# Performance work log

Hardware: AMD Instinct MI355X
Metric: run time of the kernel (lower is better)

Reference implementation:

```python
import jax, jax.numpy as jnp
import numpy as np

NUM_ROUTING = 3

def _squash(s):
    # squared_norm * s / ((1 + squared_norm) * sqrt(squared_norm)), norm over last dim
    sn = jnp.sum(s * s, axis=-1, keepdims=True)
    return sn * s / ((1.0 + sn) * jnp.sqrt(sn))

def setup_inputs() -> dict:
    key = jax.random.key(0)
    kx, kw = jax.random.split(key)
    B, IN_CAPS, IN_DIM, OUT_CAPS, OUT_DIM = 64, 8192, 8, 8, 16
    x = jax.random.normal(kx, (B, IN_CAPS, IN_DIM), dtype=jnp.float32)
    W = 0.01 * jax.random.normal(kw, (IN_CAPS, OUT_CAPS, IN_DIM, OUT_DIM), dtype=jnp.float32)
    return {"x": x, "W": W}

def reference(x, W):
    # x: [B, in_caps, in_dim]; W: [in_caps, out_caps, in_dim, out_dim]
    u_hat = jnp.einsum('ijnm,bin->bijm', W, x)          # [B, i, j, m]
    temp_u_hat = jax.lax.stop_gradient(u_hat)           # detach, routing uses no grads
    B, I, J = x.shape[0], W.shape[0], W.shape[1]
    b = jnp.zeros((B, I, J), dtype=x.dtype)
    for _ in range(NUM_ROUTING - 1):
        c = jax.nn.softmax(b, axis=2)                   # over out_caps j
        s = jnp.einsum('bij,bijm->bjm', c, temp_u_hat)  # [B, j, m]
        v = _squash(s)
        b = b + jnp.einsum('bjm,bijm->bij', v, temp_u_hat)  # agreement
    c = jax.nn.softmax(b, axis=2)
    s = jnp.einsum('bij,bijm->bjm', c, u_hat)
    return _squash(s)                                   # [B, out_caps, out_dim]
```

## Files before the change

### kernel.cpp

```cpp
#include <hip/hip_runtime.h>


#define BB      64
#define ICAPS   8192
#define NDIM    8
#define JCAPS   8
#define MDIM    16
#define NBLK    256
#define ICHUNK  (ICAPS / NBLK)
#define IG      8
#define NSTAGE  (ICHUNK / IG)
#define WJ_STRIDE (NDIM * MDIM + 4)
#define WI_STRIDE (JCAPS * WJ_STRIDE)
#define S_ELEMS  (BB * JCAPS * MDIM)

template <int MODE>
__global__ __launch_bounds__(1024, 4) void caps_pass_kernel(
    const float* __restrict__ x, const float* __restrict__ W,
    const float* __restrict__ vsum, float* __restrict__ partial)
{
    __shared__ float Wlds[IG * WI_STRIDE];

    const int tid = threadIdx.x;
    const int mq  = tid & 3;
    const int j   = (tid >> 2) & 7;
    const int bg  = tid >> 5;
    const int b0  = bg;
    const int b1  = bg + 32;
    const int blk = blockIdx.x;
    const int i0  = blk * ICHUNK;

    float s0[4] = {0.f, 0.f, 0.f, 0.f};
    float s1[4] = {0.f, 0.f, 0.f, 0.f};

    float v0[4], v1[4];
    if (MODE == 1) {
        const float4 a = *(const float4*)&vsum[(b0 * JCAPS + j) * MDIM + mq * 4];
        v0[0] = a.x; v0[1] = a.y; v0[2] = a.z; v0[3] = a.w;
        const float4 c = *(const float4*)&vsum[(b1 * JCAPS + j) * MDIM + mq * 4];
        v1[0] = c.x; v1[1] = c.y; v1[2] = c.z; v1[3] = c.w;
    }

    for (int st = 0; st < NSTAGE; ++st) {
        {
            const int iL  = tid >> 7;
            const int rem = tid & 127;
            const float4* src = (const float4*)(W + (size_t)(i0 + st * IG + iL) * 1024
                                                  + rem * 8);
            float4* dst = (float4*)&Wlds[iL * WI_STRIDE + (rem >> 4) * WJ_STRIDE
                                         + (rem & 15) * 8];
            dst[0] = src[0]; dst[1] = src[1];
        }
        __syncthreads();

        #pragma unroll
        for (int ii = 0; ii < IG; ++ii) {
            const int i = i0 + st * IG + ii;
            const float4 xa0 = *(const float4*)&x[((size_t)b0 * ICAPS + i) * NDIM];
            const float4 xb0 = *(const float4*)&x[((size_t)b0 * ICAPS + i) * NDIM + 4];
            const float4 xa1 = *(const float4*)&x[((size_t)b1 * ICAPS + i) * NDIM];
            const float4 xb1 = *(const float4*)&x[((size_t)b1 * ICAPS + i) * NDIM + 4];
            const float xs0[8] = {xa0.x, xa0.y, xa0.z, xa0.w, xb0.x, xb0.y, xb0.z, xb0.w};
            const float xs1[8] = {xa1.x, xa1.y, xa1.z, xa1.w, xb1.x, xb1.y, xb1.z, xb1.w};

            float u0[4] = {0.f, 0.f, 0.f, 0.f};
            float u1[4] = {0.f, 0.f, 0.f, 0.f};
            const float* wb = &Wlds[ii * WI_STRIDE + j * WJ_STRIDE + mq * 4];
            #pragma unroll
            for (int n = 0; n < NDIM; ++n) {
                const float4 wq = *(const float4*)&wb[n * MDIM];
                u0[0] += xs0[n] * wq.x; u0[1] += xs0[n] * wq.y;
                u0[2] += xs0[n] * wq.z; u0[3] += xs0[n] * wq.w;
                u1[0] += xs1[n] * wq.x; u1[1] += xs1[n] * wq.y;
                u1[2] += xs1[n] * wq.z; u1[3] += xs1[n] * wq.w;
            }

            if (MODE == 0) {
                #pragma unroll
                for (int m = 0; m < 4; ++m) { s0[m] += u0[m]; s1[m] += u1[m]; }
            } else {
                float lp0 = u0[0] * v0[0] + u0[1] * v0[1] + u0[2] * v0[2] + u0[3] * v0[3];
                float lp1 = u1[0] * v1[0] + u1[1] * v1[1] + u1[2] * v1[2] + u1[3] * v1[3];
                lp0 += __shfl_xor(lp0, 1);  lp0 += __shfl_xor(lp0, 2);
                lp1 += __shfl_xor(lp1, 1);  lp1 += __shfl_xor(lp1, 2);
                const float e0 = __expf(lp0);
                const float e1 = __expf(lp1);
                float d0 = e0, d1 = e1;
                d0 += __shfl_xor(d0, 4); d0 += __shfl_xor(d0, 8); d0 += __shfl_xor(d0, 16);
                d1 += __shfl_xor(d1, 4); d1 += __shfl_xor(d1, 8); d1 += __shfl_xor(d1, 16);
                const float c0 = e0 * __builtin_amdgcn_rcpf(d0);
                const float c1 = e1 * __builtin_amdgcn_rcpf(d1);
                #pragma unroll
                for (int m = 0; m < 4; ++m) { s0[m] += c0 * u0[m]; s1[m] += c1 * u1[m]; }
            }
        }
        __syncthreads();
    }

    const float sc = (MODE == 0) ? 0.125f : 1.0f;
    float* pp = partial + (size_t)blk * S_ELEMS;
    float4 o0, o1;
    o0.x = s0[0] * sc; o0.y = s0[1] * sc; o0.z = s0[2] * sc; o0.w = s0[3] * sc;
    o1.x = s1[0] * sc; o1.y = s1[1] * sc; o1.z = s1[2] * sc; o1.w = s1[3] * sc;
    *(float4*)&pp[(b0 * JCAPS + j) * MDIM + mq * 4] = o0;
    *(float4*)&pp[(b1 * JCAPS + j) * MDIM + mq * 4] = o1;
}

template <int OP>
__global__ __launch_bounds__(256) void caps_reduce_kernel(
    const float* __restrict__ partial, float* __restrict__ vsum, float* __restrict__ out)
{
    __shared__ float sd[256];
    const int bo  = blockIdx.x;
    const int tid = threadIdx.x;
    const int kg  = tid >> 6;
    const int tl  = tid & 63;
    const int t   = bo * 64 + tl;

    float a0 = 0.f, a1 = 0.f, a2 = 0.f, a3 = 0.f;
    const float* p = partial + (size_t)kg * 64 * S_ELEMS + t;
    #pragma unroll
    for (int k = 0; k < 64; k += 4) {
        a0 += p[(size_t)(k + 0) * S_ELEMS];
        a1 += p[(size_t)(k + 1) * S_ELEMS];
        a2 += p[(size_t)(k + 2) * S_ELEMS];
        a3 += p[(size_t)(k + 3) * S_ELEMS];
    }
    sd[tid] = (a0 + a1) + (a2 + a3);
    __syncthreads();

    if (tid < 64) {
        const float s = (sd[tid] + sd[64 + tid]) + (sd[128 + tid] + sd[192 + tid]);
        float sn = s * s;
        sn += __shfl_xor(sn, 1);
        sn += __shfl_xor(sn, 2);
        sn += __shfl_xor(sn, 4);
        sn += __shfl_xor(sn, 8);
        const float v = s * sqrtf(sn) / (1.f + sn);
        const int tt = bo * 64 + tid;
        if (OP == 2)      out[tt]   = v;
        else if (OP == 1) vsum[tt] += v;
        else              vsum[tt]  = v;
    }
}

extern "C" void kernel_launch(void* const* d_in, const int* in_sizes, int n_in,
                              void* d_out, int out_size, void* d_ws, size_t ws_size,
                              hipStream_t stream)
{
    const float* x = (const float*)d_in[0];
    const float* W = (const float*)d_in[1];
    float* out = (float*)d_out;

    float* partial = (float*)d_ws;
    float* vsum    = partial + (size_t)NBLK * S_ELEMS;

    caps_pass_kernel<0><<<NBLK, 1024, 0, stream>>>(x, W, vsum, partial);
    caps_reduce_kernel<0><<<128, 256, 0, stream>>>(partial, vsum, nullptr);
    caps_pass_kernel<1><<<NBLK, 1024, 0, stream>>>(x, W, vsum, partial);
    caps_reduce_kernel<1><<<128, 256, 0, stream>>>(partial, vsum, nullptr);
    caps_pass_kernel<1><<<NBLK, 1024, 0, stream>>>(x, W, vsum, partial);
    caps_reduce_kernel<2><<<128, 256, 0, stream>>>(partial, vsum, out);
}
```

Measured before the change: 207.0 us.

## Remap threads to full out_dim per (b,j) and split input capsules across halves

```diff
diff --git a/kernel.cpp b/kernel.cpp
--- a/kernel.cpp
+++ b/kernel.cpp
@@ -21,24 +21,25 @@
 {
     __shared__ float Wlds[IG * WI_STRIDE];
 
-    const int tid = threadIdx.x;
-    const int mq  = tid & 3;
-    const int j   = (tid >> 2) & 7;
-    const int bg  = tid >> 5;
-    const int b0  = bg;
-    const int b1  = bg + 32;
-    const int blk = blockIdx.x;
-    const int i0  = blk * ICHUNK;
+    const int tid  = threadIdx.x;
+    const int j    = tid & 7;
+    const int b    = (tid >> 3) & 63;
+    const int isub = tid >> 9;
+    const int blk  = blockIdx.x;
+    const int i0   = blk * ICHUNK;
 
-    float s0[4] = {0.f, 0.f, 0.f, 0.f};
-    float s1[4] = {0.f, 0.f, 0.f, 0.f};
+    float s[MDIM];
+    #pragma unroll
+    for (int m = 0; m < MDIM; ++m) s[m] = 0.f;
 
-    float v0[4], v1[4];
+    float v[MDIM];
     if (MODE == 1) {
-        const float4 a = *(const float4*)&vsum[(b0 * JCAPS + j) * MDIM + mq * 4];
-        v0[0] = a.x; v0[1] = a.y; v0[2] = a.z; v0[3] = a.w;
-        const float4 c = *(const float4*)&vsum[(b1 * JCAPS + j) * MDIM + mq * 4];
-        v1[0] = c.x; v1[1] = c.y; v1[2] = c.z; v1[3] = c.w;
+        #pragma unroll
+        for (int q = 0; q < 4; ++q) {
+            const float4 a = *(const float4*)&vsum[(b * JCAPS + j) * MDIM + q * 4];
+            v[q * 4 + 0] = a.x; v[q * 4 + 1] = a.y;
+            v[q * 4 + 2] = a.z; v[q * 4 + 3] = a.w;
+        }
     }
 
     for (int st = 0; st < NSTAGE; ++st) {
@@ -54,56 +55,79 @@
         __syncthreads();
 
         #pragma unroll
-        for (int ii = 0; ii < IG; ++ii) {
-            const int i = i0 + st * IG + ii;
-            const float4 xa0 = *(const float4*)&x[((size_t)b0 * ICAPS + i) * NDIM];
-            const float4 xb0 = *(const float4*)&x[((size_t)b0 * ICAPS + i) * NDIM + 4];
-            const float4 xa1 = *(const float4*)&x[((size_t)b1 * ICAPS + i) * NDIM];
-            const float4 xb1 = *(const float4*)&x[((size_t)b1 * ICAPS + i) * NDIM + 4];
-            const float xs0[8] = {xa0.x, xa0.y, xa0.z, xa0.w, xb0.x, xb0.y, xb0.z, xb0.w};
-            const float xs1[8] = {xa1.x, xa1.y, xa1.z, xa1.w, xb1.x, xb1.y, xb1.z, xb1.w};
+        for (int t = 0; t < IG / 2; ++t) {
+            const int ii = t * 2 + isub;
+            const int i  = i0 + st * IG + ii;
+            const float4 xa = *(const float4*)&x[((size_t)b * ICAPS + i) * NDIM];
+            const float4 xb = *(const float4*)&x[((size_t)b * ICAPS + i) * NDIM + 4];
+            const float xs[8] = {xa.x, xa.y, xa.z, xa.w, xb.x, xb.y, xb.z, xb.w};
 
-            float u0[4] = {0.f, 0.f, 0.f, 0.f};
-            float u1[4] = {0.f, 0.f, 0.f, 0.f};
-            const float* wb = &Wlds[ii * WI_STRIDE + j * WJ_STRIDE + mq * 4];
+            float u[MDIM];
+            #pragma unroll
+            for (int m = 0; m < MDIM; ++m) u[m] = 0.f;
+            const float* wb = &Wlds[ii * WI_STRIDE + j * WJ_STRIDE];
             #pragma unroll
             for (int n = 0; n < NDIM; ++n) {
-                const float4 wq = *(const float4*)&wb[n * MDIM];
-                u0[0] += xs0[n] * wq.x; u0[1] += xs0[n] * wq.y;
-                u0[2] += xs0[n] * wq.z; u0[3] += xs0[n] * wq.w;
-                u1[0] += xs1[n] * wq.x; u1[1] += xs1[n] * wq.y;
-                u1[2] += xs1[n] * wq.z; u1[3] += xs1[n] * wq.w;
+                const float4 w0 = *(const float4*)&wb[n * MDIM + 0];
+                const float4 w1 = *(const float4*)&wb[n * MDIM + 4];
+                const float4 w2 = *(const float4*)&wb[n * MDIM + 8];
+                const float4 w3 = *(const float4*)&wb[n * MDIM + 12];
+                const float xn = xs[n];
+                u[0]  += xn * w0.x; u[1]  += xn * w0.y; u[2]  += xn * w0.z; u[3]  += xn * w0.w;
+                u[4]  += xn * w1.x; u[5]  += xn * w1.y; u[6]  += xn * w1.z; u[7]  += xn * w1.w;
+                u[8]  += xn * w2.x; u[9]  += xn * w2.y; u[10] += xn * w2.z; u[11] += xn * w2.w;
+                u[12] += xn * w3.x; u[13] += xn * w3.y; u[14] += xn * w3.z; u[15] += xn * w3.w;
             }
 
             if (MODE == 0) {
                 #pragma unroll
-                for (int m = 0; m < 4; ++m) { s0[m] += u0[m]; s1[m] += u1[m]; }
+                for (int m = 0; m < MDIM; ++m) s[m] += u[m];
             } else {
-                float lp0 = u0[0] * v0[0] + u0[1] * v0[1] + u0[2] * v0[2] + u0[3] * v0[3];
-                float lp1 = u1[0] * v1[0] + u1[1] * v1[1] + u1[2] * v1[2] + u1[3] * v1[3];
-                lp0 += __shfl_xor(lp0, 1);  lp0 += __shfl_xor(lp0, 2);
-                lp1 += __shfl_xor(lp1, 1);  lp1 += __shfl_xor(lp1, 2);
-                const float e0 = __expf(lp0);
-                const float e1 = __expf(lp1);
-                float d0 = e0, d1 = e1;
-                d0 += __shfl_xor(d0, 4); d0 += __shfl_xor(d0, 8); d0 += __shfl_xor(d0, 16);
-                d1 += __shfl_xor(d1, 4); d1 += __shfl_xor(d1, 8); d1 += __shfl_xor(d1, 16);
-                const float c0 = e0 * __builtin_amdgcn_rcpf(d0);
-                const float c1 = e1 * __builtin_amdgcn_rcpf(d1);
+                float la = v[0] * u[0],  lb = v[1] * u[1];
+                float lc = v[2] * u[2],  ld = v[3] * u[3];
+                la += v[4]  * u[4];  lb += v[5]  * u[5];
+                lc += v[6]  * u[6];  ld += v[7]  * u[7];
+                la += v[8]  * u[8];  lb += v[9]  * u[9];
+                lc += v[10] * u[10]; ld += v[11] * u[11];
+                la += v[12] * u[12]; lb += v[13] * u[13];
+                lc += v[14] * u[14]; ld += v[15] * u[15];
+                const float lp = (la + lb) + (lc + ld);
+                const float e = __expf(lp);
+                float d = e;
+                d += __shfl_xor(d, 1);
+                d += __shfl_xor(d, 2);
+                d += __shfl_xor(d, 4);
+                const float c = e * __builtin_amdgcn_rcpf(d);
                 #pragma unroll
-                for (int m = 0; m < 4; ++m) { s0[m] += c0 * u0[m]; s1[m] += c1 * u1[m]; }
+                for (int m = 0; m < MDIM; ++m) s[m] += c * u[m];
             }
         }
         __syncthreads();
     }
 
-    const float sc = (MODE == 0) ? 0.125f : 1.0f;
-    float* pp = partial + (size_t)blk * S_ELEMS;
-    float4 o0, o1;
-    o0.x = s0[0] * sc; o0.y = s0[1] * sc; o0.z = s0[2] * sc; o0.w = s0[3] * sc;
-    o1.x = s1[0] * sc; o1.y = s1[1] * sc; o1.z = s1[2] * sc; o1.w = s1[3] * sc;
-    *(float4*)&pp[(b0 * JCAPS + j) * MDIM + mq * 4] = o0;
-    *(float4*)&pp[(b1 * JCAPS + j) * MDIM + mq * 4] = o1;
+    float* red = Wlds;
+    if (isub == 1) {
+        #pragma unroll
+        for (int q = 0; q < 4; ++q) {
+            float4 o;
+            o.x = s[q * 4 + 0]; o.y = s[q * 4 + 1];
+            o.z = s[q * 4 + 2]; o.w = s[q * 4 + 3];
+            *(float4*)&red[(b * JCAPS + j) * MDIM + q * 4] = o;
+        }
+    }
+    __syncthreads();
+    if (isub == 0) {
+        const float sc = (MODE == 0) ? 0.125f : 1.0f;
+        float* pp = partial + (size_t)blk * S_ELEMS + (b * JCAPS + j) * MDIM;
+        #pragma unroll
+        for (int q = 0; q < 4; ++q) {
+            const float4 r = *(const float4*)&red[(b * JCAPS + j) * MDIM + q * 4];
+            float4 o;
+            o.x = (s[q * 4 + 0] + r.x) * sc; o.y = (s[q * 4 + 1] + r.y) * sc;
+            o.z = (s[q * 4 + 2] + r.z) * sc; o.w = (s[q * 4 + 3] + r.w) * sc;
+            *(float4*)&pp[q * 4] = o;
+        }
+    }
 }
 
 template <int OP>
```

Result: faster. 192.2 us (-7.2%).
